# Kernel tuning notes

Hardware: AMD Instinct MI355X
Metric: run time of the kernel (lower is better)

## Reference

```python
import jax, jax.numpy as jnp
import numpy as np

BS, UE, RX, D = 4, 8, 128, 64
D_OUT = 64


def setup_inputs() -> dict:
    key = jax.random.key(0)
    ks = jax.random.split(key, 8)
    s1 = 1.0 / np.sqrt(5 * D)
    s2 = 1.0 / np.sqrt(D)
    return {
        "x": jax.random.normal(ks[0], (BS, UE, RX, D), dtype=jnp.float32),
        "W1": jax.random.uniform(ks[1], (D, 5 * D), jnp.float32, -s1, s1),
        "b1": jax.random.uniform(ks[2], (D,), jnp.float32, -s1, s1),
        "ln_g": jnp.ones((D,), jnp.float32),
        "ln_b": jnp.zeros((D,), jnp.float32),
        "bias": jnp.zeros((D,), jnp.float32),
        "W2": jax.random.uniform(ks[3], (D_OUT, D), jnp.float32, -s2, s2),
        "b2": jax.random.uniform(ks[4], (D_OUT,), jnp.float32, -s2, s2),
    }


def reference(x, W1, b1, ln_g, ln_b, bias, W2, b2):
    bs, ue, rx, d = x.shape
    # diagonal mask [rx, rx, 1] broadcast over feature dim
    diag = jnp.eye(rx, dtype=x.dtype)[:, :, None]
    m = jnp.mean(x, axis=2, keepdims=True)          # [bs, ue, 1, d]
    # Five pairwise feature maps, each [bs, ue, rx, rx, d]
    x1 = x[:, :, :, None, :] * diag                 # diag_embed(x)
    x2 = jnp.broadcast_to(x[:, :, :, None, :], (bs, ue, rx, rx, d))  # row copy
    x3 = jnp.broadcast_to(x[:, :, None, :, :], (bs, ue, rx, rx, d))  # col copy
    x4 = m[:, :, :, None, :] * diag                 # diag_embed(mean)
    x5 = jnp.broadcast_to(m[:, :, :, None, :], (bs, ue, rx, rx, d))  # mean bcast
    xAll = jnp.concatenate([x1, x2, x3, x4, x5], axis=-1)  # [bs, ue, rx, rx, 5d]
    # fc1
    h = jnp.einsum("buijf,df->buijd", xAll, W1) + b1
    # LayerNorm over last dim (eps = 1e-5, torch default)
    mu = jnp.mean(h, axis=-1, keepdims=True)
    var = jnp.mean(jnp.square(h - mu), axis=-1, keepdims=True)
    h = (h - mu) * jax.lax.rsqrt(var + 1e-5) * ln_g + ln_b
    y = jax.nn.relu(h)
    # diagonal-masked learned bias
    y = y + bias * diag
    # fc2
    out = jnp.einsum("buijd,od->buijo", y, W2) + b2
    return out
```

## Files before the change

kernel.cpp:

```cpp
#include <hip/hip_runtime.h>
#include <stdint.h>

#define RX 128
#define ROWS 4096
#define NBU 32

typedef __attribute__((ext_vector_type(8))) short short8;
typedef __attribute__((ext_vector_type(4))) float f32x4;

#define WS_R1 0
#define WS_R2 262144
#define WS_R3 524288
#define WS_R4 786432
#define WS_R5 788480

#define LDP 68

__device__ __forceinline__ short bf16rne(float f) {
    uint32_t u = __float_as_uint(f);
    u += 0x7FFFu + ((u >> 16) & 1u);
    return (short)(u >> 16);
}

__device__ __forceinline__ void ld16f(const float* __restrict__ p, int d0, int d1,
                                      float* __restrict__ o) {
    *(float4*)(o + 0)  = *(const float4*)(p + d0);
    *(float4*)(o + 4)  = *(const float4*)(p + d0 + 4);
    *(float4*)(o + 8)  = *(const float4*)(p + d1);
    *(float4*)(o + 12) = *(const float4*)(p + d1 + 4);
}

__global__ __launch_bounds__(192) void k_pre(const float* __restrict__ x,
                                             const float* __restrict__ W1,
                                             const float* __restrict__ b1,
                                             float* __restrict__ ws) {
    __shared__ float s[8256];
    const int t = threadIdx.x;
    const int blk = blockIdx.x;

    if (blk < 512) {
        const int r0 = blk * 8;
        if (t < 128)
            ((float4*)s)[t] = ((const float4*)(x + r0 * 64))[t];
        __syncthreads();
        const int arr = t >> 6;
        const int dp  = t & 63;
        const float* wrow = W1 + dp * 320 + arr * 64;
        float4 w[16];
#pragma unroll
        for (int fc = 0; fc < 16; ++fc) w[fc] = ((const float4*)wrow)[fc];
        float* dst = ws + (arr == 0 ? WS_R1 : arr == 1 ? WS_R2 : WS_R3);
#pragma unroll
        for (int r = 0; r < 8; ++r) {
            float acc = 0.f;
#pragma unroll
            for (int fc = 0; fc < 16; ++fc) {
                float4 xv = ((const float4*)(s + r * 64))[fc];
                acc = fmaf(xv.x, w[fc].x, acc);
                acc = fmaf(xv.y, w[fc].y, acc);
                acc = fmaf(xv.z, w[fc].z, acc);
                acc = fmaf(xv.w, w[fc].w, acc);
            }
            dst[(r0 + r) * 64 + dp] = acc;
        }
    } else {
        const int bu = blk - 512;
        const float* xb = x + bu * RX * 64;
        for (int idx = t; idx < 2048; idx += 192)
            ((float4*)s)[idx] = ((const float4*)xb)[idx];
        __syncthreads();
        if (t < 64) {
            float a0 = 0, a1 = 0, a2 = 0, a3 = 0;
            for (int r = 0; r < 128; r += 4) {
                a0 += s[(r + 0) * 64 + t];
                a1 += s[(r + 1) * 64 + t];
                a2 += s[(r + 2) * 64 + t];
                a3 += s[(r + 3) * 64 + t];
            }
            s[8192 + t] = (a0 + a1 + a2 + a3) * (1.0f / 128.0f);
        }
        __syncthreads();
        if (t < 128) {
            const int dp = t & 63, which = t >> 6;
            const float* wrow = W1 + dp * 320 + 192 + which * 64;
            float acc = which ? b1[dp] : 0.f;
#pragma unroll
            for (int fc = 0; fc < 16; ++fc) {
                float4 mv = ((const float4*)(s + 8192))[fc];
                float4 wv = ((const float4*)wrow)[fc];
                acc = fmaf(mv.x, wv.x, acc);
                acc = fmaf(mv.y, wv.y, acc);
                acc = fmaf(mv.z, wv.z, acc);
                acc = fmaf(mv.w, wv.w, acc);
            }
            (ws + (which ? WS_R5 : WS_R4))[bu * 64 + dp] = acc;
        }
    }
}

__global__ __launch_bounds__(256) void k_main(const float* __restrict__ ws,
                                              const float* __restrict__ ln_g,
                                              const float* __restrict__ ln_b,
                                              const float* __restrict__ bias,
                                              const float* __restrict__ W2,
                                              const float* __restrict__ b2,
                                              float* __restrict__ out) {
    const float* R1  = ws + WS_R1;
    const float* R2  = ws + WS_R2;
    const float* R3  = ws + WS_R3;
    const float* r4  = ws + WS_R4;
    const float* r5b = ws + WS_R5;

    __shared__ float sR3[128 * LDP];

    const int t    = threadIdx.x;
    const int lane = t & 63;
    const int wid  = t >> 6;
    const int q    = lane >> 4;
    const int ml   = lane & 15;
    const int bu   = blockIdx.x >> 5;
    const int i0   = (blockIdx.x & 31) * 4;

    const int d0 = q * 8;
    const int d1 = 32 + q * 8;

    {
        const float* r3g = R3 + (size_t)bu * 8192;
#pragma unroll
        for (int c = 0; c < 8; ++c) {
            const int g = c * 256 + t;
            const int r = g >> 4, col = (g & 15) << 2;
            *(float4*)&sR3[r * LDP + col] = ((const float4*)r3g)[g];
        }
    }

    float r5v[16], gv[16], bbv[16];
    ld16f(r5b + bu * 64, d0, d1, r5v);
    ld16f(ln_g, d0, d1, gv);
    ld16f(ln_b, d0, d1, bbv);

    short8 bf[4][2];
#pragma unroll
    for (int ot = 0; ot < 4; ++ot) {
#pragma unroll
        for (int kt = 0; kt < 2; ++kt) {
            const float* wp = W2 + (ot * 16 + ml) * 64 + kt * 32 + q * 8;
            float4 w0 = *(const float4*)wp;
            float4 w1 = *(const float4*)(wp + 4);
            short8 v;
            v[0] = bf16rne(w0.x); v[1] = bf16rne(w0.y);
            v[2] = bf16rne(w0.z); v[3] = bf16rne(w0.w);
            v[4] = bf16rne(w1.x); v[5] = bf16rne(w1.y);
            v[6] = bf16rne(w1.z); v[7] = bf16rne(w1.w);
            bf[ot][kt] = v;
        }
    }
    float b2v[4];
#pragma unroll
    for (int ot = 0; ot < 4; ++ot) b2v[ot] = b2[ot * 16 + ml];

    __syncthreads();

#pragma unroll
    for (int ip = 0; ip < 4; ++ip) {
        const int i   = i0 + ip;
        const int row = bu * 128 + i;
        const int it  = i >> 4, im = i & 15;

        float basev[16];
        ld16f(R2 + (size_t)row * 64, d0, d1, basev);
#pragma unroll
        for (int s = 0; s < 16; ++s) basev[s] += r5v[s];

        float* outB = out + (size_t)row * 8192;

#pragma unroll
        for (int p = 0; p < 2; ++p) {
            const int jt = p * 4 + wid;
            const int j  = jt * 16 + ml;

            float h[16];
            {
                const float* sp = sR3 + j * LDP;
                *(float4*)(h + 0)  = *(const float4*)(sp + d0);
                *(float4*)(h + 4)  = *(const float4*)(sp + d0 + 4);
                *(float4*)(h + 8)  = *(const float4*)(sp + d1);
                *(float4*)(h + 12) = *(const float4*)(sp + d1 + 4);
            }
#pragma unroll
            for (int s = 0; s < 16; ++s) h[s] += basev[s];

            const bool diag = (jt == it) && (ml == im);
            if (diag) {
                float da[16], db[16];
                ld16f(R1 + (size_t)row * 64, d0, d1, da);
                ld16f(r4 + bu * 64, d0, d1, db);
#pragma unroll
                for (int s = 0; s < 16; ++s) h[s] += da[s] + db[s];
            }

            float sum = 0.f, ss = 0.f;
#pragma unroll
            for (int s = 0; s < 16; ++s) { sum += h[s]; ss = fmaf(h[s], h[s], ss); }
            sum += __shfl_xor(sum, 16); sum += __shfl_xor(sum, 32);
            ss  += __shfl_xor(ss, 16);  ss  += __shfl_xor(ss, 32);
            const float mu  = sum * 0.015625f;
            const float var = ss * 0.015625f - mu * mu;
            const float inv = rsqrtf(var + 1e-5f);

            float y[16];
#pragma unroll
            for (int s = 0; s < 16; ++s) {
                float v = fmaf((h[s] - mu) * inv, gv[s], bbv[s]);
                y[s] = fmaxf(v, 0.f);
            }
            if (diag) {
                float bi[16];
                ld16f(bias, d0, d1, bi);
#pragma unroll
                for (int s = 0; s < 16; ++s) y[s] += bi[s];
            }

            short8 a0, a1;
#pragma unroll
            for (int jj = 0; jj < 8; ++jj) { a0[jj] = bf16rne(y[jj]); a1[jj] = bf16rne(y[8 + jj]); }

#pragma unroll
            for (int ot = 0; ot < 4; ++ot) {
                f32x4 acc = { b2v[ot], b2v[ot], b2v[ot], b2v[ot] };
                acc = __builtin_amdgcn_mfma_f32_16x16x32_bf16(a0, bf[ot][0], acc, 0, 0, 0);
                acc = __builtin_amdgcn_mfma_f32_16x16x32_bf16(a1, bf[ot][1], acc, 0, 0, 0);
                float* ob = outB + (size_t)(jt * 16 + q * 4) * 64 + ot * 16 + ml;
                ob[0]   = acc[0];
                ob[64]  = acc[1];
                ob[128] = acc[2];
                ob[192] = acc[3];
            }
        }
    }
}

extern "C" void kernel_launch(void* const* d_in, const int* in_sizes, int n_in,
                              void* d_out, int out_size, void* d_ws, size_t ws_size,
                              hipStream_t stream) {
    const float* x    = (const float*)d_in[0];
    const float* W1   = (const float*)d_in[1];
    const float* b1   = (const float*)d_in[2];
    const float* ln_g = (const float*)d_in[3];
    const float* ln_b = (const float*)d_in[4];
    const float* bias = (const float*)d_in[5];
    const float* W2   = (const float*)d_in[6];
    const float* b2   = (const float*)d_in[7];
    float* ws  = (float*)d_ws;
    float* out = (float*)d_out;

    hipLaunchKernelGGL(k_pre, dim3(544), dim3(192), 0, stream, x, W1, b1, ws);
    hipLaunchKernelGGL(k_main, dim3(1024), dim3(256), 0, stream,
                       ws, ln_g, ln_b, bias, W2, b2, out);
}
```

Measured before the change: 167.9 us.

## Swap MFMA operands for vectorized output stores and use hardware bf16 pack

Swaps the A/B operands of the MFMA so each lane's accumulator holds four consecutive output columns of one row. The results can then go out as single 16-byte stores instead of four strided scalar stores, and the bias is loaded as a vector to match. Software bf16 rounding is replaced by the v_cvt_pk_bf16_f32 instruction. The LayerNorm affine is folded into fmas, the per-block r5 values are reloaded inside the loop to free registers, and launch bounds now request 3 blocks per CU for occupancy.

```diff
diff --git a/kernel.cpp b/kernel.cpp
--- a/kernel.cpp
+++ b/kernel.cpp
@@ -2,7 +2,6 @@
 #include <stdint.h>
 
 #define RX 128
-#define ROWS 4096
 #define NBU 32
 
 typedef __attribute__((ext_vector_type(8))) short short8;
@@ -16,10 +15,21 @@
 
 #define LDP 68
 
-__device__ __forceinline__ short bf16rne(float f) {
-    uint32_t u = __float_as_uint(f);
-    u += 0x7FFFu + ((u >> 16) & 1u);
-    return (short)(u >> 16);
+__device__ __forceinline__ uint32_t cvtpk(float a, float b) {
+    uint32_t r;
+    asm("v_cvt_pk_bf16_f32 %0, %1, %2" : "=v"(r) : "v"(a), "v"(b));
+    return r;
+}
+
+union S8U4 { short8 s8; uint32_t u[4]; };
+
+__device__ __forceinline__ short8 pack8(const float* __restrict__ y) {
+    S8U4 t;
+    t.u[0] = cvtpk(y[0], y[1]);
+    t.u[1] = cvtpk(y[2], y[3]);
+    t.u[2] = cvtpk(y[4], y[5]);
+    t.u[3] = cvtpk(y[6], y[7]);
+    return t.s8;
 }
 
 __device__ __forceinline__ void ld16f(const float* __restrict__ p, int d0, int d1,
@@ -98,13 +108,13 @@
     }
 }
 
-__global__ __launch_bounds__(256) void k_main(const float* __restrict__ ws,
-                                              const float* __restrict__ ln_g,
-                                              const float* __restrict__ ln_b,
-                                              const float* __restrict__ bias,
-                                              const float* __restrict__ W2,
-                                              const float* __restrict__ b2,
-                                              float* __restrict__ out) {
+__global__ __launch_bounds__(256, 3) void k_main(const float* __restrict__ ws,
+                                                 const float* __restrict__ ln_g,
+                                                 const float* __restrict__ ln_b,
+                                                 const float* __restrict__ bias,
+                                                 const float* __restrict__ W2,
+                                                 const float* __restrict__ b2,
+                                                 float* __restrict__ out) {
     const float* R1  = ws + WS_R1;
     const float* R2  = ws + WS_R2;
     const float* R3  = ws + WS_R3;
@@ -134,8 +144,7 @@
         }
     }
 
-    float r5v[16], gv[16], bbv[16];
-    ld16f(r5b + bu * 64, d0, d1, r5v);
+    float gv[16], bbv[16];
     ld16f(ln_g, d0, d1, gv);
     ld16f(ln_b, d0, d1, bbv);
 
@@ -147,17 +156,18 @@
             const float* wp = W2 + (ot * 16 + ml) * 64 + kt * 32 + q * 8;
             float4 w0 = *(const float4*)wp;
             float4 w1 = *(const float4*)(wp + 4);
-            short8 v;
-            v[0] = bf16rne(w0.x); v[1] = bf16rne(w0.y);
-            v[2] = bf16rne(w0.z); v[3] = bf16rne(w0.w);
-            v[4] = bf16rne(w1.x); v[5] = bf16rne(w1.y);
-            v[6] = bf16rne(w1.z); v[7] = bf16rne(w1.w);
-            bf[ot][kt] = v;
-        }
-    }
-    float b2v[4];
-#pragma unroll
-    for (int ot = 0; ot < 4; ++ot) b2v[ot] = b2[ot * 16 + ml];
+            S8U4 v;
+            v.u[0] = cvtpk(w0.x, w0.y);
+            v.u[1] = cvtpk(w0.z, w0.w);
+            v.u[2] = cvtpk(w1.x, w1.y);
+            v.u[3] = cvtpk(w1.z, w1.w);
+            bf[ot][kt] = v.s8;
+        }
+    }
+    f32x4 b2q[4];
+#pragma unroll
+    for (int ot = 0; ot < 4; ++ot)
+        b2q[ot] = *(const f32x4*)(b2 + ot * 16 + q * 4);
 
     __syncthreads();
 
@@ -167,10 +177,11 @@
         const int row = bu * 128 + i;
         const int it  = i >> 4, im = i & 15;
 
-        float basev[16];
+        float basev[16], tv[16];
         ld16f(R2 + (size_t)row * 64, d0, d1, basev);
-#pragma unroll
-        for (int s = 0; s < 16; ++s) basev[s] += r5v[s];
+        ld16f(r5b + bu * 64, d0, d1, tv);
+#pragma unroll
+        for (int s = 0; s < 16; ++s) basev[s] += tv[s];
 
         float* outB = out + (size_t)row * 8192;
 
@@ -207,34 +218,30 @@
             const float mu  = sum * 0.015625f;
             const float var = ss * 0.015625f - mu * mu;
             const float inv = rsqrtf(var + 1e-5f);
-
-            float y[16];
+            const float nmi = -mu * inv;
+
 #pragma unroll
             for (int s = 0; s < 16; ++s) {
-                float v = fmaf((h[s] - mu) * inv, gv[s], bbv[s]);
-                y[s] = fmaxf(v, 0.f);
+                float v = fmaf(fmaf(h[s], inv, nmi), gv[s], bbv[s]);
+                h[s] = fmaxf(v, 0.f);
             }
             if (diag) {
                 float bi[16];
                 ld16f(bias, d0, d1, bi);
 #pragma unroll
-                for (int s = 0; s < 16; ++s) y[s] += bi[s];
-            }
-
-            short8 a0, a1;
-#pragma unroll
-            for (int jj = 0; jj < 8; ++jj) { a0[jj] = bf16rne(y[jj]); a1[jj] = bf16rne(y[8 + jj]); }
-
+                for (int s = 0; s < 16; ++s) h[s] += bi[s];
+            }
+
+            const short8 a0 = pack8(h);
+            const short8 a1 = pack8(h + 8);
+
+            float* ob = outB + (size_t)j * 64 + q * 4;
 #pragma unroll
             for (int ot = 0; ot < 4; ++ot) {
-                f32x4 acc = { b2v[ot], b2v[ot], b2v[ot], b2v[ot] };
-                acc = __builtin_amdgcn_mfma_f32_16x16x32_bf16(a0, bf[ot][0], acc, 0, 0, 0);
-                acc = __builtin_amdgcn_mfma_f32_16x16x32_bf16(a1, bf[ot][1], acc, 0, 0, 0);
-                float* ob = outB + (size_t)(jt * 16 + q * 4) * 64 + ot * 16 + ml;
-                ob[0]   = acc[0];
-                ob[64]  = acc[1];
-                ob[128] = acc[2];
-                ob[192] = acc[3];
+                f32x4 acc = b2q[ot];
+                acc = __builtin_amdgcn_mfma_f32_16x16x32_bf16(bf[ot][0], a0, acc, 0, 0, 0);
+                acc = __builtin_amdgcn_mfma_f32_16x16x32_bf16(bf[ot][1], a1, acc, 0, 0, 0);
+                *(f32x4*)(ob + ot * 16) = acc;
             }
         }
     }
```

New measurement: 176.1 us. 1.05x slower.
